# Kernel tuning notes

Hardware: AMD Instinct MI355X
Metric: run time of the kernel (lower is better)

## Reference

```python
import jax, jax.numpy as jnp
import jax.scipy.linalg as jsp
import numpy as np

# Problem dimensions (match init_kwargs P_shape/A_shape)
N = 256   # variables
M = 512   # constraints
B = 64    # batch

# OSQP ADMM hyper-parameters (fixed-rho variant of the OSQP algorithm)
SIGMA = 1e-6
RHO = 0.1
ALPHA = 1.6
N_ITERS = 500


def setup_inputs() -> dict:
    key = jax.random.key(0)
    kP, kq, kA, kc = jax.random.split(key, 4)
    # P is diagonal with strictly positive entries -> PSD (values are the nnz of P)
    P_val = jax.random.uniform(kP, (B, N), dtype=jnp.float32) + 0.1
    q_val = jax.random.normal(kq, (B, N), dtype=jnp.float32)
    # A is a dense pattern; values stored row-major as its nnz vector
    A_val = jax.random.normal(kA, (B, M * N), dtype=jnp.float32) / np.sqrt(N)
    # Feasible box: l <= u by construction
    center = jax.random.normal(kc, (B, M), dtype=jnp.float32)
    l_val = center - 1.0
    u_val = center + 1.0
    return {"P_val": P_val, "q_val": q_val, "A_val": A_val, "l_val": l_val, "u_val": u_val}


def _admm_qp(P_val, q_val, A_val, l_val, u_val):
    """Batched OSQP-style ADMM solve of min 1/2 x'Px + q'x  s.t. l <= Ax <= u.

    P is diagonal (nnz pattern = diag), A is dense (nnz pattern = full m x n).
    """
    A = A_val.reshape(B, M, N)                      # [B,m,n]
    # KKT-like matrix M_k = P + sigma*I + rho*A'A   [B,n,n]
    eye = jnp.eye(N, dtype=P_val.dtype)
    P_diag = P_val + SIGMA                          # diagonal of P + sigma*I
    Mk = RHO * jnp.einsum('bmi,bmj->bij', A, A) + jax.vmap(jnp.diag)(P_diag)
    L = jnp.linalg.cholesky(Mk)                     # [B,n,n], factor once, reuse
    Lt = jnp.swapaxes(L, -1, -2)

    def kkt_solve(rhs):                             # rhs [B,n]
        y1 = jsp.solve_triangular(L, rhs[..., None], lower=True)
        y2 = jsp.solve_triangular(Lt, y1, lower=False)
        return y2[..., 0]

    x0 = jnp.zeros((B, N), dtype=P_val.dtype)
    z0 = jnp.zeros((B, M), dtype=P_val.dtype)
    y0 = jnp.zeros((B, M), dtype=P_val.dtype)

    def step(state, _):
        x, z, y = state
        rhs = SIGMA * x - q_val + jnp.einsum('bmn,bm->bn', A, RHO * z - y)
        x_t = kkt_solve(rhs)                        # x-tilde
        z_t = jnp.einsum('bmn,bn->bm', A, x_t)      # z-tilde = A x_t
        x_new = ALPHA * x_t + (1.0 - ALPHA) * x
        z_hat = ALPHA * z_t + (1.0 - ALPHA) * z
        z_new = jnp.clip(z_hat + y / RHO, l_val, u_val)
        y_new = y + RHO * (z_hat - z_new)
        return (x_new, z_new, y_new), None

    (x, _, _), _ = jax.lax.scan(step, (x0, z0, y0), None, length=N_ITERS)
    return x


def reference(P_val, q_val, A_val, l_val, u_val):
    return _admm_qp(P_val, q_val, A_val, l_val, u_val)   # [B, n] primal solutions
```

## Files before the change

### kernel.cpp

```cpp
#include <hip/hip_runtime.h>
#include <hip/hip_fp16.h>

#define N_VAR 256
#define M_CON 512
#define BATCH 64
#define SIGMA_C 1e-6f
#define RHO_C 0.1f
#define ALPHA_C 1.6f
#define NITERS 500

__global__ __launch_bounds__(256) void k_transpose(const float* __restrict__ A,
                                                   float* __restrict__ At) {
  __shared__ float tile[32][33];
  int b = blockIdx.z;
  int n0 = blockIdx.x * 32;
  int m0 = blockIdx.y * 32;
  const float* Ab = A + (size_t)b * (M_CON * N_VAR);
  float* Atb = At + (size_t)b * (M_CON * N_VAR);
  int tx = threadIdx.x, ty = threadIdx.y;
#pragma unroll
  for (int j = 0; j < 32; j += 8)
    tile[ty + j][tx] = Ab[(size_t)(m0 + ty + j) * N_VAR + n0 + tx];
  __syncthreads();
#pragma unroll
  for (int j = 0; j < 32; j += 8)
    Atb[(size_t)(n0 + ty + j) * M_CON + m0 + tx] = tile[tx][ty + j];
}

__global__ __launch_bounds__(256) void k_ntgemm(
    const float* __restrict__ X, const float* __restrict__ Y,
    float* __restrict__ C, int I, int J, int K,
    long long bsX, long long bsY, long long bsC, float alpha,
    const float* __restrict__ diagv, int tilesJ) {
  int b = blockIdx.y;
  int ti = blockIdx.x / tilesJ, tj = blockIdx.x % tilesJ;
  int i0 = ti * 128, j0 = tj * 128;
  const float* Xb = X + (size_t)b * bsX;
  const float* Yb = Y + (size_t)b * bsY;
  float* Cb = C + (size_t)b * bsC;
  __shared__ float Xs[16][128];
  __shared__ float Ys[16][128];
  int tid = threadIdx.x;
  int tx = tid & 15, ty = tid >> 4;
  float acc[8][8];
#pragma unroll
  for (int r = 0; r < 8; ++r)
#pragma unroll
    for (int c = 0; c < 8; ++c) acc[r][c] = 0.0f;

  for (int kk = 0; kk < K; kk += 16) {
#pragma unroll
    for (int v = 0; v < 2; ++v) {
      int idx = v * 256 + tid;
      int row = idx >> 2;
      int k4 = (idx & 3) * 4;
      float4 gx = *(const float4*)(Xb + (size_t)(i0 + row) * K + kk + k4);
      Xs[k4 + 0][row] = gx.x; Xs[k4 + 1][row] = gx.y;
      Xs[k4 + 2][row] = gx.z; Xs[k4 + 3][row] = gx.w;
      float4 gy = *(const float4*)(Yb + (size_t)(j0 + row) * K + kk + k4);
      Ys[k4 + 0][row] = gy.x; Ys[k4 + 1][row] = gy.y;
      Ys[k4 + 2][row] = gy.z; Ys[k4 + 3][row] = gy.w;
    }
    __syncthreads();
#pragma unroll
    for (int k = 0; k < 16; ++k) {
      float xr[8], yr[8];
      *(float4*)&xr[0] = *(float4*)&Xs[k][ty * 8];
      *(float4*)&xr[4] = *(float4*)&Xs[k][ty * 8 + 4];
      *(float4*)&yr[0] = *(float4*)&Ys[k][tx * 8];
      *(float4*)&yr[4] = *(float4*)&Ys[k][tx * 8 + 4];
#pragma unroll
      for (int r = 0; r < 8; ++r)
#pragma unroll
        for (int c = 0; c < 8; ++c) acc[r][c] += xr[r] * yr[c];
    }
    __syncthreads();
  }
#pragma unroll
  for (int r = 0; r < 8; ++r) {
    int gi = i0 + ty * 8 + r;
#pragma unroll
    for (int c = 0; c < 8; ++c) {
      int gj = j0 + tx * 8 + c;
      float val = acc[r][c] * alpha;
      if (diagv != nullptr && gi == gj) val += diagv[(size_t)b * N_VAR + gi] + SIGMA_C;
      Cb[(size_t)gi * J + gj] = val;
    }
  }
}

__global__ __launch_bounds__(512, 2) void k_invert(const float* __restrict__ Mk,
                                                   float* __restrict__ Mi) {
  int b = blockIdx.x;
  const float* src = Mk + (size_t)b * 65536;
  float* dst = Mi + (size_t)b * 65536;
  int t = threadIdx.x;
  int c = t & 255, rh = t >> 8;

  float a[128];
#pragma unroll
  for (int j = 0; j < 128; ++j) a[j] = src[(size_t)(rh * 128 + j) * 256 + c];

  __shared__ float colPan[256][8];
  __shared__ float rowPan[2][8][260];
  __shared__ float PiSh[64];
  __shared__ float Rp[8][260];

  int rh_s = __builtin_amdgcn_readfirstlane(rh);
  int cw_s = __builtin_amdgcn_readfirstlane((t >> 6) & 3);

  if (rh == 0) {
#pragma unroll
    for (int j = 0; j < 8; ++j) rowPan[0][j][c] = a[j];
  }
  __syncthreads();

  for (int s = 0; s < 32; ++s) {
    int kb = s * 8;
    int cur = s & 1, nxt = cur ^ 1;
    int kh = kb >> 7, kj = kb & 127;
    int khn = (kb + 8) >> 7, kjn = (kb + 8) & 127;
    bool mycol = (c >= kb) && (c < kb + 8);

    if (cw_s == (kb >> 6)) {
      if (mycol) {
        int f = c - kb;
#pragma unroll
        for (int j = 0; j < 128; ++j) colPan[rh * 128 + j][f] = a[j];
      }
    }
    if (t < 64) {
      int e = t >> 3, f = t & 7;
      float p = rowPan[cur][e][kb + f];
#pragma unroll
      for (int k2 = 0; k2 < 8; ++k2) {
        float piv = __shfl(p, k2 * 8 + k2);
        float rv = __shfl(p, k2 * 8 + f);
        float cv = __shfl(p, e * 8 + k2);
        float pivinv = 1.0f / piv;
        float srv = rv * pivinv;
        float gen = p - cv * srv;
        p = gen;
        if (e == k2) p = srv;
        if (f == k2) p = -cv * pivinv;
        if (e == k2 && f == k2) p = pivinv;
      }
      PiSh[t] = p;
    }
    __syncthreads();

    float rpan[8];
#pragma unroll
    for (int f2 = 0; f2 < 8; ++f2) rpan[f2] = rowPan[cur][f2][c];
    float rp[8];
#pragma unroll
    for (int e = 0; e < 8; ++e) {
      float4 p0 = *(const float4*)&PiSh[e * 8];
      float4 p1 = *(const float4*)&PiSh[e * 8 + 4];
      rp[e] = p0.x * rpan[0] + p0.y * rpan[1] + p0.z * rpan[2] + p0.w * rpan[3] +
              p1.x * rpan[4] + p1.y * rpan[5] + p1.z * rpan[6] + p1.w * rpan[7];
    }
    if (cw_s == (kb >> 6)) {
      if (mycol) {
        int f = c - kb;
#pragma unroll
        for (int e = 0; e < 8; ++e) rp[e] = PiSh[e * 8 + f];
      }
    }
#pragma unroll
    for (int e = 0; e < 8; ++e) Rp[e][c] = rp[e];

    bool myhalfk = (rh_s == kh);
    bool stashw = (s != 31) && (rh_s == khn);
#pragma unroll
    for (int j = 0; j < 128; ++j) {
      float4 c0 = *(const float4*)&colPan[rh * 128 + j][0];
      float4 c1 = *(const float4*)&colPan[rh * 128 + j][4];
      float aold = a[j];
      float nv = aold -
                 (c0.x * rp[0] + c0.y * rp[1] + c0.z * rp[2] + c0.w * rp[3] +
                  c1.x * rp[4] + c1.y * rp[5] + c1.z * rp[6] + c1.w * rp[7]);
      if (mycol) nv -= aold;
      if (myhalfk && j >= kj && j < kj + 8)
        nv = Rp[j - kj][c];
      a[j] = nv;
      if (stashw && j >= kjn && j < kjn + 8)
        rowPan[nxt][j - kjn][c] = nv;
    }
    __syncthreads();
  }

#pragma unroll
  for (int j = 0; j < 128; ++j) dst[(size_t)(rh * 128 + j) * 256 + c] = a[j];
}

__global__ __launch_bounds__(256) void k_matvec_h(const float* __restrict__ Mi,
                                                  const float* __restrict__ q,
                                                  float* __restrict__ h) {
  int b = blockIdx.x, t = threadIdx.x;
  __shared__ float qs[256];
  qs[t] = q[(size_t)b * 256 + t];
  __syncthreads();
  const float* Mb = Mi + (size_t)b * 65536;
  float acc = 0.0f;
  for (int k = 0; k < 256; ++k) acc += Mb[(size_t)k * 256 + t] * qs[k];
  h[(size_t)b * 256 + t] = acc;
}

__global__ __launch_bounds__(512) void k_matvec_d(const float* __restrict__ At,
                                                  const float* __restrict__ h,
                                                  float* __restrict__ d) {
  int b = blockIdx.x, t = threadIdx.x;
  __shared__ float hs[256];
  if (t < 256) hs[t] = h[(size_t)b * 256 + t];
  __syncthreads();
  const float* Ab = At + (size_t)b * 131072;
  float acc = 0.0f;
  for (int n = 0; n < 256; ++n) acc += Ab[(size_t)n * 512 + t] * hs[n];
  d[(size_t)b * 512 + t] = acc;
}

__global__ __launch_bounds__(512, 2) void k_admm4(
    const float* __restrict__ G, const float* __restrict__ dvec,
    const float* __restrict__ lv, const float* __restrict__ uv,
    unsigned long long* __restrict__ wtag, float* __restrict__ Sbuf) {
  int g = blockIdx.x;
  int b = (g & 7) + 8 * ((g >> 3) & 7);
  int s = g >> 6;
  int t = threadIdx.x;
  int l = t & 63, wv = t >> 6;
  int c0 = wv * 64;

  __shared__ __align__(16) float wloc[512];
  __shared__ float part[8][128];

  const float* Gb = G + (size_t)b * 262144;
  const float* g0p = Gb + (size_t)(s * 128 + l) * 512 + c0;
  const float* g1p = Gb + (size_t)(s * 128 + 64 + l) * 512 + c0;
  float G0[64], G1[64];
#pragma unroll
  for (int j = 0; j < 16; ++j) {
    float4 v0 = *(const float4*)(g0p + 4 * j);
    G0[4 * j + 0] = v0.x; G0[4 * j + 1] = v0.y;
    G0[4 * j + 2] = v0.z; G0[4 * j + 3] = v0.w;
    float4 v1 = *(const float4*)(g1p + 4 * j);
    G1[4 * j + 0] = v1.x; G1[4 * j + 1] = v1.y;
    G1[4 * j + 2] = v1.z; G1[4 * j + 3] = v1.w;
  }

  float zreg = 0.0f, yreg = 0.0f, Sreg = 0.0f;
  float lreg = 0.0f, ureg = 0.0f, dreg = 0.0f;
  if (t < 128) {
    lreg = lv[(size_t)b * 512 + s * 128 + t];
    ureg = uv[(size_t)b * 512 + s * 128 + t];
    dreg = dvec[(size_t)b * 512 + s * 128 + t];
  }
  wloc[t] = 0.0f;

  unsigned long long* wt0 = wtag + (size_t)b * 512;
  unsigned long long* wt1 = wtag + 32768 + (size_t)b * 512;
  int gr = (s * 128 + t) & 511;
  const float4* wq4 = (const float4*)(wloc + c0);

  for (int it = 0; it < NITERS; ++it) {
    __syncthreads();

    float r0a = 0.f, r0b = 0.f, r1a = 0.f, r1b = 0.f;
#pragma unroll
    for (int j = 0; j < 8; ++j) {
      float4 wa = wq4[2 * j];
      float4 wc = wq4[2 * j + 1];
      r0a += G0[8 * j + 0] * wa.x + G0[8 * j + 1] * wa.y +
             G0[8 * j + 2] * wa.z + G0[8 * j + 3] * wa.w;
      r1a += G1[8 * j + 0] * wa.x + G1[8 * j + 1] * wa.y +
             G1[8 * j + 2] * wa.z + G1[8 * j + 3] * wa.w;
      r0b += G0[8 * j + 4] * wc.x + G0[8 * j + 5] * wc.y +
             G0[8 * j + 6] * wc.z + G0[8 * j + 7] * wc.w;
      r1b += G1[8 * j + 4] * wc.x + G1[8 * j + 5] * wc.y +
             G1[8 * j + 6] * wc.z + G1[8 * j + 7] * wc.w;
    }
    part[wv][l] = r0a + r0b;
    part[wv][64 + l] = r1a + r1b;
    __syncthreads();

    if (t < 128) {
      float w_old = RHO_C * zreg - yreg;
      Sreg = w_old - 0.6f * Sreg;
      float p = part[0][t] + part[1][t] + part[2][t] + part[3][t] +
                part[4][t] + part[5][t] + part[6][t] + part[7][t];
      float zt = p - dreg;
      float zh = ALPHA_C * zt + (1.0f - ALPHA_C) * zreg;
      float zc = zh + yreg * (1.0f / RHO_C);
      zc = fminf(fmaxf(zc, lreg), ureg);
      yreg += RHO_C * (zh - zc);
      zreg = zc;
      float wn = RHO_C * zreg - yreg;
      wloc[s * 128 + t] = wn;
      if (it < NITERS - 1) {
        unsigned long long pk =
            ((unsigned long long)(unsigned)(it + 1) << 32) |
            (unsigned long long)__float_as_uint(wn);
        unsigned long long* wp = ((it + 1) & 1) ? wt1 : wt0;
        __hip_atomic_store(&wp[s * 128 + t], pk, __ATOMIC_RELAXED,
                           __HIP_MEMORY_SCOPE_AGENT);
      }
    } else if (it < NITERS - 1) {
      unsigned long long* wp = ((it + 1) & 1) ? wt1 : wt0;
      unsigned want = (unsigned)(it + 1);
      unsigned long long v;
      for (;;) {
        v = __hip_atomic_load(&wp[gr], __ATOMIC_RELAXED,
                              __HIP_MEMORY_SCOPE_AGENT);
        if ((unsigned)(v >> 32) == want) break;
        __builtin_amdgcn_s_sleep(1);
      }
      wloc[gr] = __uint_as_float((unsigned)(v & 0xffffffffu));
    }
  }

  if (t < 128) Sbuf[(size_t)b * 512 + s * 128 + t] = Sreg;
}

__global__ __launch_bounds__(256) void k_final(
    const float* __restrict__ A, const float* __restrict__ q,
    const float* __restrict__ Mi, const float* __restrict__ Sbuf,
    float* __restrict__ xout) {
  int b = blockIdx.x, t = threadIdx.x;
  __shared__ float Ssh[512];
  __shared__ float uu[256];
  for (int i = t; i < 512; i += 256) Ssh[i] = Sbuf[(size_t)b * 512 + i];
  __syncthreads();
  const float* Ab = A + (size_t)b * 131072;
  float acc = 0.0f;
  for (int m = 0; m < 512; ++m) acc += Ab[(size_t)m * 256 + t] * Ssh[m];
  uu[t] = ALPHA_C * acc - q[(size_t)b * 256 + t];
  __syncthreads();
  const float* Mb = Mi + (size_t)b * 65536;
  float x = 0.0f;
  for (int kk = 0; kk < 256; ++kk) x += Mb[(size_t)kk * 256 + t] * uu[kk];
  xout[(size_t)b * 256 + t] = x;
}

extern "C" void kernel_launch(void* const* d_in, const int* in_sizes, int n_in,
                              void* d_out, int out_size, void* d_ws, size_t ws_size,
                              hipStream_t stream) {
  (void)in_sizes; (void)n_in; (void)out_size; (void)ws_size;
  const float* P = (const float*)d_in[0];
  const float* q = (const float*)d_in[1];
  const float* Av = (const float*)d_in[2];
  const float* lv = (const float*)d_in[3];
  const float* uv = (const float*)d_in[4];
  float* xout = (float*)d_out;

  float* ws = (float*)d_ws;
  float* At = ws;
  float* F  = ws;
  float* Mi = ws + 8388608;
  float* Mk = ws + 12582912;
  float* G  = ws + 12582912;
  float* hv = ws + 29360128;
  float* dv = ws + 29376512;
  float* Sbuf = ws + 29409280;
  unsigned long long* wtag = (unsigned long long*)ws;

  k_transpose<<<dim3(8, 16, 64), dim3(32, 8), 0, stream>>>(Av, At);
  k_ntgemm<<<dim3(4, 64), 256, 0, stream>>>(At, At, Mk, 256, 256, 512,
                                            131072LL, 131072LL, 65536LL,
                                            RHO_C, P, 2);
  k_invert<<<64, 512, 0, stream>>>(Mk, Mi);
  k_matvec_h<<<64, 256, 0, stream>>>(Mi, q, hv);
  k_matvec_d<<<64, 512, 0, stream>>>(At, hv, dv);
  k_ntgemm<<<dim3(8, 64), 256, 0, stream>>>(Av, Mi, F, 512, 256, 256,
                                            131072LL, 65536LL, 131072LL,
                                            1.0f, nullptr, 2);
  k_ntgemm<<<dim3(16, 64), 256, 0, stream>>>(F, Av, G, 512, 512, 256,
                                             131072LL, 131072LL, 262144LL,
                                             1.0f, nullptr, 4);
  k_admm4<<<256, 512, 0, stream>>>(G, dv, lv, uv, wtag, Sbuf);
  k_final<<<64, 256, 0, stream>>>(Av, q, Mi, Sbuf, xout);
}
```

Baseline: 1.629 ms.

## Split each batch across eight blocks and interleave two batches per block

The persistent ADMM kernel now assigns each block 64 rows of two different batch problems instead of 128 rows of one problem, so every batch is spread across eight blocks. The block alternates between the two batches, so the global-memory exchange of one batch's w vector can overlap with the matvec of the other. This is meant to hide inter-block synchronisation latency, but each batch now waits on more peers per iteration and there are more barriers per iteration.

Result: slower. 1.858 ms (+14.0%).

```diff
diff --git a/kernel.cpp b/kernel.cpp
--- a/kernel.cpp
+++ b/kernel.cpp
@@ -220,105 +220,148 @@
   d[(size_t)b * 512 + t] = acc;
 }
 
-__global__ __launch_bounds__(512, 2) void k_admm4(
+__global__ __launch_bounds__(512, 2) void k_admm8(
     const float* __restrict__ G, const float* __restrict__ dvec,
     const float* __restrict__ lv, const float* __restrict__ uv,
     unsigned long long* __restrict__ wtag, float* __restrict__ Sbuf) {
   int g = blockIdx.x;
-  int b = (g & 7) + 8 * ((g >> 3) & 7);
-  int s = g >> 6;
+  int p = g & 31;
+  int s = g >> 5;
+  int b0 = 2 * p, b1 = 2 * p + 1;
   int t = threadIdx.x;
   int l = t & 63, wv = t >> 6;
   int c0 = wv * 64;
-
-  __shared__ __align__(16) float wloc[512];
-  __shared__ float part[8][128];
-
-  const float* Gb = G + (size_t)b * 262144;
-  const float* g0p = Gb + (size_t)(s * 128 + l) * 512 + c0;
-  const float* g1p = Gb + (size_t)(s * 128 + 64 + l) * 512 + c0;
-  float G0[64], G1[64];
+  int row = s * 64 + l;
+
+  __shared__ __align__(16) float wlA[512], wlB[512];
+  __shared__ float pA[8][64], pB[8][64];
+
+  const float* gAp = G + (size_t)b0 * 262144 + (size_t)row * 512 + c0;
+  const float* gBp = G + (size_t)b1 * 262144 + (size_t)row * 512 + c0;
+  float GA[64], GB[64];
 #pragma unroll
   for (int j = 0; j < 16; ++j) {
-    float4 v0 = *(const float4*)(g0p + 4 * j);
-    G0[4 * j + 0] = v0.x; G0[4 * j + 1] = v0.y;
-    G0[4 * j + 2] = v0.z; G0[4 * j + 3] = v0.w;
-    float4 v1 = *(const float4*)(g1p + 4 * j);
-    G1[4 * j + 0] = v1.x; G1[4 * j + 1] = v1.y;
-    G1[4 * j + 2] = v1.z; G1[4 * j + 3] = v1.w;
-  }
-
-  float zreg = 0.0f, yreg = 0.0f, Sreg = 0.0f;
-  float lreg = 0.0f, ureg = 0.0f, dreg = 0.0f;
-  if (t < 128) {
-    lreg = lv[(size_t)b * 512 + s * 128 + t];
-    ureg = uv[(size_t)b * 512 + s * 128 + t];
-    dreg = dvec[(size_t)b * 512 + s * 128 + t];
-  }
-  wloc[t] = 0.0f;
-
-  unsigned long long* wt0 = wtag + (size_t)b * 512;
-  unsigned long long* wt1 = wtag + 32768 + (size_t)b * 512;
-  int gr = (s * 128 + t) & 511;
-  const float4* wq4 = (const float4*)(wloc + c0);
+    float4 va = *(const float4*)(gAp + 4 * j);
+    GA[4 * j + 0] = va.x; GA[4 * j + 1] = va.y;
+    GA[4 * j + 2] = va.z; GA[4 * j + 3] = va.w;
+    float4 vb = *(const float4*)(gBp + 4 * j);
+    GB[4 * j + 0] = vb.x; GB[4 * j + 1] = vb.y;
+    GB[4 * j + 2] = vb.z; GB[4 * j + 3] = vb.w;
+  }
+
+  float zA = 0, yA = 0, SA = 0, lA = 0, uA = 0, dA = 0;
+  float zB = 0, yB = 0, SB = 0, lB = 0, uB = 0, dB = 0;
+  if (t < 64) {
+    int m = s * 64 + t;
+    lA = lv[(size_t)b0 * 512 + m]; uA = uv[(size_t)b0 * 512 + m];
+    dA = dvec[(size_t)b0 * 512 + m];
+    lB = lv[(size_t)b1 * 512 + m]; uB = uv[(size_t)b1 * 512 + m];
+    dB = dvec[(size_t)b1 * 512 + m];
+  }
+  wlA[t] = 0.0f;
+  wlB[t] = 0.0f;
+
+  unsigned long long* A0 = wtag + (size_t)b0 * 512;
+  unsigned long long* A1 = wtag + 32768 + (size_t)b0 * 512;
+  unsigned long long* B0 = wtag + (size_t)b1 * 512;
+  unsigned long long* B1 = wtag + 32768 + (size_t)b1 * 512;
+  int pr = (s * 64 + 64 + (t - 64)) & 511;
+
+  const float4* wqA = (const float4*)(wlA + c0);
+  const float4* wqB = (const float4*)(wlB + c0);
 
   for (int it = 0; it < NITERS; ++it) {
     __syncthreads();
-
-    float r0a = 0.f, r0b = 0.f, r1a = 0.f, r1b = 0.f;
-#pragma unroll
-    for (int j = 0; j < 8; ++j) {
-      float4 wa = wq4[2 * j];
-      float4 wc = wq4[2 * j + 1];
-      r0a += G0[8 * j + 0] * wa.x + G0[8 * j + 1] * wa.y +
-             G0[8 * j + 2] * wa.z + G0[8 * j + 3] * wa.w;
-      r1a += G1[8 * j + 0] * wa.x + G1[8 * j + 1] * wa.y +
-             G1[8 * j + 2] * wa.z + G1[8 * j + 3] * wa.w;
-      r0b += G0[8 * j + 4] * wc.x + G0[8 * j + 5] * wc.y +
-             G0[8 * j + 6] * wc.z + G0[8 * j + 7] * wc.w;
-      r1b += G1[8 * j + 4] * wc.x + G1[8 * j + 5] * wc.y +
-             G1[8 * j + 6] * wc.z + G1[8 * j + 7] * wc.w;
-    }
-    part[wv][l] = r0a + r0b;
-    part[wv][64 + l] = r1a + r1b;
-    __syncthreads();
-
-    if (t < 128) {
-      float w_old = RHO_C * zreg - yreg;
-      Sreg = w_old - 0.6f * Sreg;
-      float p = part[0][t] + part[1][t] + part[2][t] + part[3][t] +
-                part[4][t] + part[5][t] + part[6][t] + part[7][t];
-      float zt = p - dreg;
-      float zh = ALPHA_C * zt + (1.0f - ALPHA_C) * zreg;
-      float zc = zh + yreg * (1.0f / RHO_C);
-      zc = fminf(fmaxf(zc, lreg), ureg);
-      yreg += RHO_C * (zh - zc);
-      zreg = zc;
-      float wn = RHO_C * zreg - yreg;
-      wloc[s * 128 + t] = wn;
-      if (it < NITERS - 1) {
-        unsigned long long pk =
-            ((unsigned long long)(unsigned)(it + 1) << 32) |
-            (unsigned long long)__float_as_uint(wn);
-        unsigned long long* wp = ((it + 1) & 1) ? wt1 : wt0;
-        __hip_atomic_store(&wp[s * 128 + t], pk, __ATOMIC_RELAXED,
+    bool more = (it < NITERS - 1);
+    unsigned want = (unsigned)(it + 1);
+
+    float accA = 0.0f;
+#pragma unroll
+    for (int j = 0; j < 16; ++j) {
+      float4 w4 = wqA[j];
+      accA += GA[4 * j + 0] * w4.x + GA[4 * j + 1] * w4.y +
+              GA[4 * j + 2] * w4.z + GA[4 * j + 3] * w4.w;
+    }
+    pA[wv][l] = accA;
+    __syncthreads();
+
+    if (t < 64) {
+      float w_old = RHO_C * zA - yA;
+      SA = w_old - 0.6f * SA;
+      float zt = pA[0][t] + pA[1][t] + pA[2][t] + pA[3][t] +
+                 pA[4][t] + pA[5][t] + pA[6][t] + pA[7][t] - dA;
+      float zh = ALPHA_C * zt + (1.0f - ALPHA_C) * zA;
+      float zc = fminf(fmaxf(zh + yA * (1.0f / RHO_C), lA), uA);
+      yA += RHO_C * (zh - zc);
+      zA = zc;
+      float wn = RHO_C * zA - yA;
+      wlA[s * 64 + t] = wn;
+      if (more) {
+        unsigned long long pk = ((unsigned long long)want << 32) |
+                                (unsigned long long)__float_as_uint(wn);
+        unsigned long long* wp = ((it + 1) & 1) ? A1 : A0;
+        __hip_atomic_store(&wp[s * 64 + t], pk, __ATOMIC_RELAXED,
                            __HIP_MEMORY_SCOPE_AGENT);
       }
-    } else if (it < NITERS - 1) {
-      unsigned long long* wp = ((it + 1) & 1) ? wt1 : wt0;
-      unsigned want = (unsigned)(it + 1);
+    }
+    float accB = 0.0f;
+#pragma unroll
+    for (int j = 0; j < 16; ++j) {
+      float4 w4 = wqB[j];
+      accB += GB[4 * j + 0] * w4.x + GB[4 * j + 1] * w4.y +
+              GB[4 * j + 2] * w4.z + GB[4 * j + 3] * w4.w;
+    }
+    pB[wv][l] = accB;
+    __syncthreads();
+
+    if (t < 64) {
+      float w_old = RHO_C * zB - yB;
+      SB = w_old - 0.6f * SB;
+      float zt = pB[0][t] + pB[1][t] + pB[2][t] + pB[3][t] +
+                 pB[4][t] + pB[5][t] + pB[6][t] + pB[7][t] - dB;
+      float zh = ALPHA_C * zt + (1.0f - ALPHA_C) * zB;
+      float zc = fminf(fmaxf(zh + yB * (1.0f / RHO_C), lB), uB);
+      yB += RHO_C * (zh - zc);
+      zB = zc;
+      float wn = RHO_C * zB - yB;
+      wlB[s * 64 + t] = wn;
+      if (more) {
+        unsigned long long pk = ((unsigned long long)want << 32) |
+                                (unsigned long long)__float_as_uint(wn);
+        unsigned long long* wp = ((it + 1) & 1) ? B1 : B0;
+        __hip_atomic_store(&wp[s * 64 + t], pk, __ATOMIC_RELAXED,
+                           __HIP_MEMORY_SCOPE_AGENT);
+      }
+    } else if (more) {
+      unsigned long long* wp = ((it + 1) & 1) ? A1 : A0;
       unsigned long long v;
       for (;;) {
-        v = __hip_atomic_load(&wp[gr], __ATOMIC_RELAXED,
+        v = __hip_atomic_load(&wp[pr], __ATOMIC_RELAXED,
                               __HIP_MEMORY_SCOPE_AGENT);
         if ((unsigned)(v >> 32) == want) break;
         __builtin_amdgcn_s_sleep(1);
       }
-      wloc[gr] = __uint_as_float((unsigned)(v & 0xffffffffu));
-    }
-  }
-
-  if (t < 128) Sbuf[(size_t)b * 512 + s * 128 + t] = Sreg;
+      wlA[pr] = __uint_as_float((unsigned)(v & 0xffffffffu));
+    }
+    __syncthreads();
+
+    if (more && t >= 64) {
+      unsigned long long* wp = ((it + 1) & 1) ? B1 : B0;
+      unsigned long long v;
+      for (;;) {
+        v = __hip_atomic_load(&wp[pr], __ATOMIC_RELAXED,
+                              __HIP_MEMORY_SCOPE_AGENT);
+        if ((unsigned)(v >> 32) == want) break;
+        __builtin_amdgcn_s_sleep(1);
+      }
+      wlB[pr] = __uint_as_float((unsigned)(v & 0xffffffffu));
+    }
+  }
+
+  if (t < 64) {
+    Sbuf[(size_t)b0 * 512 + s * 64 + t] = SA;
+    Sbuf[(size_t)b1 * 512 + s * 64 + t] = SB;
+  }
 }
 
 __global__ __launch_bounds__(256) void k_final(
@@ -376,6 +419,6 @@
   k_ntgemm<<<dim3(16, 64), 256, 0, stream>>>(F, Av, G, 512, 512, 256,
                                              131072LL, 131072LL, 262144LL,
                                              1.0f, nullptr, 4);
-  k_admm4<<<256, 512, 0, stream>>>(G, dv, lv, uv, wtag, Sbuf);
+  k_admm8<<<256, 512, 0, stream>>>(G, dv, lv, uv, wtag, Sbuf);
   k_final<<<64, 256, 0, stream>>>(Av, q, Mi, Sbuf, xout);
 }
```

## Exploit symmetry in Gram GEMMs and double-buffer shared tiles in ntgemm

Applied to the files above, without the earlier changes.

The A'A and A·Mi·A' GEMMs now compute only the upper-triangular 128x128 tiles (3 of 4, and 10 of 16). A new mirror kernel then copies the lower-triangle 32x32 blocks from their transposes. The GEMM kernel also double-buffers its shared-memory tiles, prefetching the next K slice into registers while computing on the current one. This cuts FLOPs in the setup GEMMs at the cost of extra mirror launches, and doubles shared memory per block.

New measurement: 1.742 ms. +6.9%, slower.

```diff
diff --git a/kernel.cpp b/kernel.cpp
--- a/kernel.cpp
+++ b/kernel.cpp
@@ -29,53 +29,78 @@
 
 __global__ __launch_bounds__(256) void k_ntgemm(
     const float* __restrict__ X, const float* __restrict__ Y,
-    float* __restrict__ C, int I, int J, int K,
+    float* __restrict__ C, int J, int K,
     long long bsX, long long bsY, long long bsC, float alpha,
-    const float* __restrict__ diagv, int tilesJ) {
+    const float* __restrict__ diagv, int tilesJ, int symN) {
   int b = blockIdx.y;
-  int ti = blockIdx.x / tilesJ, tj = blockIdx.x % tilesJ;
+  int ti, tj;
+  if (symN > 0) {
+    int r = blockIdx.x;
+    ti = 0;
+    while (r >= symN - ti) { r -= (symN - ti); ++ti; }
+    tj = ti + r;
+  } else {
+    ti = blockIdx.x / tilesJ;
+    tj = blockIdx.x % tilesJ;
+  }
   int i0 = ti * 128, j0 = tj * 128;
   const float* Xb = X + (size_t)b * bsX;
   const float* Yb = Y + (size_t)b * bsY;
   float* Cb = C + (size_t)b * bsC;
-  __shared__ float Xs[16][128];
-  __shared__ float Ys[16][128];
+  __shared__ float Xs[2][16][128];
+  __shared__ float Ys[2][16][128];
   int tid = threadIdx.x;
   int tx = tid & 15, ty = tid >> 4;
+  int row0 = tid >> 2, k40 = (tid & 3) * 4;
+
   float acc[8][8];
 #pragma unroll
   for (int r = 0; r < 8; ++r)
 #pragma unroll
     for (int c = 0; c < 8; ++c) acc[r][c] = 0.0f;
 
-  for (int kk = 0; kk < K; kk += 16) {
-#pragma unroll
-    for (int v = 0; v < 2; ++v) {
-      int idx = v * 256 + tid;
-      int row = idx >> 2;
-      int k4 = (idx & 3) * 4;
-      float4 gx = *(const float4*)(Xb + (size_t)(i0 + row) * K + kk + k4);
-      Xs[k4 + 0][row] = gx.x; Xs[k4 + 1][row] = gx.y;
-      Xs[k4 + 2][row] = gx.z; Xs[k4 + 3][row] = gx.w;
-      float4 gy = *(const float4*)(Yb + (size_t)(j0 + row) * K + kk + k4);
-      Ys[k4 + 0][row] = gy.x; Ys[k4 + 1][row] = gy.y;
-      Ys[k4 + 2][row] = gy.z; Ys[k4 + 3][row] = gy.w;
-    }
-    __syncthreads();
+  float4 rx0, rx1, ry0, ry1;
+  auto prefetch = [&](int kk) {
+    rx0 = *(const float4*)(Xb + (size_t)(i0 + row0) * K + kk + k40);
+    rx1 = *(const float4*)(Xb + (size_t)(i0 + row0 + 64) * K + kk + k40);
+    ry0 = *(const float4*)(Yb + (size_t)(j0 + row0) * K + kk + k40);
+    ry1 = *(const float4*)(Yb + (size_t)(j0 + row0 + 64) * K + kk + k40);
+  };
+  auto commit = [&](int buf) {
+    Xs[buf][k40 + 0][row0] = rx0.x; Xs[buf][k40 + 1][row0] = rx0.y;
+    Xs[buf][k40 + 2][row0] = rx0.z; Xs[buf][k40 + 3][row0] = rx0.w;
+    Xs[buf][k40 + 0][row0 + 64] = rx1.x; Xs[buf][k40 + 1][row0 + 64] = rx1.y;
+    Xs[buf][k40 + 2][row0 + 64] = rx1.z; Xs[buf][k40 + 3][row0 + 64] = rx1.w;
+    Ys[buf][k40 + 0][row0] = ry0.x; Ys[buf][k40 + 1][row0] = ry0.y;
+    Ys[buf][k40 + 2][row0] = ry0.z; Ys[buf][k40 + 3][row0] = ry0.w;
+    Ys[buf][k40 + 0][row0 + 64] = ry1.x; Ys[buf][k40 + 1][row0 + 64] = ry1.y;
+    Ys[buf][k40 + 2][row0 + 64] = ry1.z; Ys[buf][k40 + 3][row0 + 64] = ry1.w;
+  };
+
+  int nkt = K >> 4;
+  prefetch(0);
+  commit(0);
+  __syncthreads();
+
+  for (int kt = 0; kt < nkt; ++kt) {
+    int cur = kt & 1;
+    if (kt + 1 < nkt) prefetch((kt + 1) * 16);
 #pragma unroll
     for (int k = 0; k < 16; ++k) {
       float xr[8], yr[8];
-      *(float4*)&xr[0] = *(float4*)&Xs[k][ty * 8];
-      *(float4*)&xr[4] = *(float4*)&Xs[k][ty * 8 + 4];
-      *(float4*)&yr[0] = *(float4*)&Ys[k][tx * 8];
-      *(float4*)&yr[4] = *(float4*)&Ys[k][tx * 8 + 4];
+      *(float4*)&xr[0] = *(float4*)&Xs[cur][k][ty * 8];
+      *(float4*)&xr[4] = *(float4*)&Xs[cur][k][ty * 8 + 4];
+      *(float4*)&yr[0] = *(float4*)&Ys[cur][k][tx * 8];
+      *(float4*)&yr[4] = *(float4*)&Ys[cur][k][tx * 8 + 4];
 #pragma unroll
       for (int r = 0; r < 8; ++r)
 #pragma unroll
         for (int c = 0; c < 8; ++c) acc[r][c] += xr[r] * yr[c];
     }
+    if (kt + 1 < nkt) commit(cur ^ 1);
     __syncthreads();
   }
+
 #pragma unroll
   for (int r = 0; r < 8; ++r) {
     int gi = i0 + ty * 8 + r;
@@ -87,6 +112,25 @@
       Cb[(size_t)gi * J + gj] = val;
     }
   }
+}
+
+__global__ __launch_bounds__(256) void k_mirror(float* __restrict__ C, int n,
+                                                long long bsC) {
+  __shared__ float tile[32][33];
+  int b = blockIdx.y;
+  int idx = blockIdx.x;
+  int bi = 1;
+  while (idx >= bi) { idx -= bi; ++bi; }
+  int bj = idx;
+  float* Cb = C + (size_t)b * bsC;
+  int tx = threadIdx.x & 31, ty = threadIdx.x >> 5;
+#pragma unroll
+  for (int j = 0; j < 32; j += 8)
+    tile[ty + j][tx] = Cb[(size_t)(bj * 32 + ty + j) * n + bi * 32 + tx];
+  __syncthreads();
+#pragma unroll
+  for (int j = 0; j < 32; j += 8)
+    Cb[(size_t)(bi * 32 + ty + j) * n + bj * 32 + tx] = tile[tx][ty + j];
 }
 
 __global__ __launch_bounds__(512, 2) void k_invert(const float* __restrict__ Mk,
@@ -364,18 +408,20 @@
   unsigned long long* wtag = (unsigned long long*)ws;
 
   k_transpose<<<dim3(8, 16, 64), dim3(32, 8), 0, stream>>>(Av, At);
-  k_ntgemm<<<dim3(4, 64), 256, 0, stream>>>(At, At, Mk, 256, 256, 512,
+  k_ntgemm<<<dim3(3, 64), 256, 0, stream>>>(At, At, Mk, 256, 512,
                                             131072LL, 131072LL, 65536LL,
-                                            RHO_C, P, 2);
+                                            RHO_C, P, 0, 2);
+  k_mirror<<<dim3(28, 64), 256, 0, stream>>>(Mk, 256, 65536LL);
   k_invert<<<64, 512, 0, stream>>>(Mk, Mi);
   k_matvec_h<<<64, 256, 0, stream>>>(Mi, q, hv);
   k_matvec_d<<<64, 512, 0, stream>>>(At, hv, dv);
-  k_ntgemm<<<dim3(8, 64), 256, 0, stream>>>(Av, Mi, F, 512, 256, 256,
+  k_ntgemm<<<dim3(8, 64), 256, 0, stream>>>(Av, Mi, F, 256, 256,
                                             131072LL, 65536LL, 131072LL,
-                                            1.0f, nullptr, 2);
-  k_ntgemm<<<dim3(16, 64), 256, 0, stream>>>(F, Av, G, 512, 512, 256,
+                                            1.0f, nullptr, 2, 0);
+  k_ntgemm<<<dim3(10, 64), 256, 0, stream>>>(F, Av, G, 512, 256,
                                              131072LL, 131072LL, 262144LL,
-                                             1.0f, nullptr, 4);
+                                             1.0f, nullptr, 0, 4);
+  k_mirror<<<dim3(120, 64), 256, 0, stream>>>(G, 512, 262144LL);
   k_admm4<<<256, 512, 0, stream>>>(G, dv, lv, uv, wtag, Sbuf);
   k_final<<<64, 256, 0, stream>>>(Av, q, Mi, Sbuf, xout);
 }
```
